# Kernel optimization log

Hardware: AMD Instinct MI355X
Metric: run time of the kernel (lower is better)

The kernel has to match this reference:

```python
import jax, jax.numpy as jnp
import numpy as np

B, N, C, OUT, K2 = 64, 4096, 64, 64, 4  # batch, lattice sites, in/out features, kersize^2

def setup_inputs() -> dict:
    key = jax.random.key(0)
    k1, k2, k3, k4 = jax.random.split(key, 4)
    std = 0.5 / jnp.sqrt(K2 * (C + OUT))  # matches module's init stddev (W_scale=b_scale=1)
    x = jax.random.normal(k1, (B, N, C), dtype=jnp.float32)
    W = jax.random.normal(k2, (K2, C, OUT), dtype=jnp.float32) * std
    b = jax.random.normal(k3, (OUT,), dtype=jnp.float32) * std
    kernel2 = jax.random.randint(k4, (N, K2), 0, N, dtype=jnp.int32)
    return {"x": x, "W": W, "b": b, "kernel2": kernel2}

def reference(x, W, b, kernel2):
    # gather neighbors: [B, N, K2, C]; contract (K2, C) with W -> [B, N, OUT]
    y = jnp.einsum('bnkc,kco->bno', x[:, kernel2, :], W)
    # bias broadcast (original used tensordot with ones([B,N]))
    return y + b
```

## Files before the change

### kernel.cpp

```cpp
#include <hip/hip_runtime.h>
#include <stdint.h>


#define N_SITES   4096
#define C_DIM     64
#define OUT_DIM   64
#define LDS_STRIDE 264

typedef __attribute__((ext_vector_type(8))) short bf16x8;
typedef __attribute__((ext_vector_type(4))) float f32x4;

__device__ __forceinline__ uint32_t pack2_bf16(float f0, float f1) {
    uint32_t u0 = __float_as_uint(f0) + 0x8000u;
    uint32_t u1 = __float_as_uint(f1) + 0x8000u;
    return __builtin_amdgcn_perm(u1, u0, 0x07060302u);
}

__global__ __launch_bounds__(256, 3)
void conv_mfma_kernel(const float* __restrict__ x, const float* __restrict__ W,
                      const float* __restrict__ bias, const int* __restrict__ kernel2,
                      float* __restrict__ out)
{
    __shared__ __align__(16) short wt[OUT_DIM * LDS_STRIDE];

    const int tid = threadIdx.x;
    const int bi  = blockIdx.x;

    const int strip = (bi & 7) + ((bi >= 2048) ? 8 : 0);
    const int group = (bi & 2047) >> 3;
    const int n0 = group * 16;
    const int b0 = strip * 4;

    const int wave = tid >> 6;
    const int lane = tid & 63;
    const int q = lane >> 4;
    const int c = lane & 15;
    const int sl = c >> 2;
    const int b  = b0 + (c & 3);

    const int n = n0 + wave * 4 + sl;
    const int4 idx = *(const int4*)(kernel2 + n * 4);
    const float* xb = x + (size_t)b * (N_SITES * C_DIM);
    const float* rp[4] = {
        xb + (size_t)idx.x * C_DIM,
        xb + (size_t)idx.y * C_DIM,
        xb + (size_t)idx.z * C_DIM,
        xb + (size_t)idx.w * C_DIM
    };

    f32x4 pay[16];
    #pragma unroll
    for (int s = 0; s < 8; ++s) {
        const float* p = rp[s >> 1] + (s & 1) * 32 + q * 8;
        pay[2*s]     = *(const f32x4*)(p);
        pay[2*s + 1] = *(const f32x4*)(p + 4);
    }

    f32x4 bias_r[4];
    #pragma unroll
    for (int t = 0; t < 4; ++t) bias_r[t] = *(const f32x4*)&bias[t*16 + q*4];

    __builtin_amdgcn_sched_barrier(0);

    {
        const int o      = tid & 63;
        const int kkbase = (tid >> 6) * 64;
        uint32_t* dst = (uint32_t*)&wt[o * LDS_STRIDE + kkbase];
        #pragma unroll
        for (int j = 0; j < 32; ++j) {
            float f0 = W[(size_t)(kkbase + 2*j    ) * OUT_DIM + o];
            float f1 = W[(size_t)(kkbase + 2*j + 1) * OUT_DIM + o];
            dst[j] = pack2_bf16(f0, f1);
        }
    }
    __syncthreads();

    f32x4 acc[4];
    #pragma unroll
    for (int t = 0; t < 4; ++t) acc[t] = (f32x4){0.f, 0.f, 0.f, 0.f};

    #pragma unroll
    for (int s = 0; s < 8; ++s) {
        bf16x8 bfrag;
        uint32_t* bp = (uint32_t*)&bfrag;
        bp[0] = pack2_bf16(pay[2*s][0],   pay[2*s][1]);
        bp[1] = pack2_bf16(pay[2*s][2],   pay[2*s][3]);
        bp[2] = pack2_bf16(pay[2*s+1][0], pay[2*s+1][1]);
        bp[3] = pack2_bf16(pay[2*s+1][2], pay[2*s+1][3]);

        const int col = s*32 + q*8;
        #pragma unroll
        for (int t = 0; t < 4; ++t) {
            bf16x8 a = *(const bf16x8*)&wt[(t*16 + c) * LDS_STRIDE + col];
            acc[t] = __builtin_amdgcn_mfma_f32_16x16x32_bf16(a, bfrag, acc[t], 0, 0, 0);
        }
    }

    float* op = out + ((size_t)b * N_SITES + n) * OUT_DIM + q * 4;
    #pragma unroll
    for (int t = 0; t < 4; ++t) {
        f32x4 v;
        #pragma unroll
        for (int r = 0; r < 4; ++r) v[r] = acc[t][r] + bias_r[t][r];
        *(f32x4*)(op + t * 16) = v;
    }
}

extern "C" void kernel_launch(void* const* d_in, const int* in_sizes, int n_in,
                              void* d_out, int out_size, void* d_ws, size_t ws_size,
                              hipStream_t stream) {
    const float* x       = (const float*)d_in[0];
    const float* W       = (const float*)d_in[1];
    const float* bias    = (const float*)d_in[2];
    const int*   kernel2 = (const int*)d_in[3];
    float* out = (float*)d_out;

    conv_mfma_kernel<<<4096, 256, 0, stream>>>(x, W, bias, kernel2, out);
}
```

Baseline: 154.3 us.

## Process four site groups per block with software-pipelined gather loads

Each block now handles 64 sites in four phases instead of 16, which amortizes the per-block W-to-bf16 LDS staging over four times more work and cuts the grid to 1024 blocks. Within each phase, the gather loads for the next half-tile are issued while the current half's MFMAs run, double-buffering through packed registers. Occupancy hint rises from 3 to 4 blocks per CU. The trade-off is fewer blocks for latency hiding and more register pressure from the pipelined payload.

```diff
diff --git a/kernel.cpp b/kernel.cpp
--- a/kernel.cpp
+++ b/kernel.cpp
@@ -6,6 +6,7 @@
 #define C_DIM     64
 #define OUT_DIM   64
 #define LDS_STRIDE 264
+#define P_PHASES  4
 
 typedef __attribute__((ext_vector_type(8))) short bf16x8;
 typedef __attribute__((ext_vector_type(4))) float f32x4;
@@ -16,7 +17,7 @@
     return __builtin_amdgcn_perm(u1, u0, 0x07060302u);
 }
 
-__global__ __launch_bounds__(256, 3)
+__global__ __launch_bounds__(256, 4)
 void conv_mfma_kernel(const float* __restrict__ x, const float* __restrict__ W,
                       const float* __restrict__ bias, const int* __restrict__ kernel2,
                       float* __restrict__ out)
@@ -26,41 +27,20 @@
     const int tid = threadIdx.x;
     const int bi  = blockIdx.x;
 
-    const int strip = (bi & 7) + ((bi >= 2048) ? 8 : 0);
-    const int group = (bi & 2047) >> 3;
-    const int n0 = group * 16;
-    const int b0 = strip * 4;
+    const int strip = (bi & 7) + ((bi >= 512) ? 8 : 0);
+    const int g     = (bi & 511) >> 3;
+    const int n0    = g * 64;
 
     const int wave = tid >> 6;
     const int lane = tid & 63;
-    const int q = lane >> 4;
-    const int c = lane & 15;
+    const int q  = lane >> 4;
+    const int c  = lane & 15;
     const int sl = c >> 2;
-    const int b  = b0 + (c & 3);
+    const int b  = strip * 4 + (c & 3);
 
-    const int n = n0 + wave * 4 + sl;
-    const int4 idx = *(const int4*)(kernel2 + n * 4);
-    const float* xb = x + (size_t)b * (N_SITES * C_DIM);
-    const float* rp[4] = {
-        xb + (size_t)idx.x * C_DIM,
-        xb + (size_t)idx.y * C_DIM,
-        xb + (size_t)idx.z * C_DIM,
-        xb + (size_t)idx.w * C_DIM
-    };
+    const int nbase = n0 + wave * 4 + sl;
 
-    f32x4 pay[16];
-    #pragma unroll
-    for (int s = 0; s < 8; ++s) {
-        const float* p = rp[s >> 1] + (s & 1) * 32 + q * 8;
-        pay[2*s]     = *(const f32x4*)(p);
-        pay[2*s + 1] = *(const f32x4*)(p + 4);
-    }
-
-    f32x4 bias_r[4];
-    #pragma unroll
-    for (int t = 0; t < 4; ++t) bias_r[t] = *(const f32x4*)&bias[t*16 + q*4];
-
-    __builtin_amdgcn_sched_barrier(0);
+    int4 idx = *(const int4*)(kernel2 + nbase * 4);
 
     {
         const int o      = tid & 63;
@@ -73,36 +53,99 @@
             dst[j] = pack2_bf16(f0, f1);
         }
     }
+
+    f32x4 bias_r[4];
+    #pragma unroll
+    for (int t = 0; t < 4; ++t) bias_r[t] = *(const f32x4*)&bias[t*16 + q*4];
+
+    const float* xq = x + (size_t)b * (N_SITES * C_DIM) + q * 8;
+
+    f32x4    pay[8];
+    uint32_t pk[16];
+    uint32_t off[4];
+
+    auto build_off = [&](int4 v) {
+        off[0] = (uint32_t)v.x * C_DIM; off[1] = (uint32_t)v.y * C_DIM;
+        off[2] = (uint32_t)v.z * C_DIM; off[3] = (uint32_t)v.w * C_DIM;
+    };
+    auto load_half = [&](int h) {
+        #pragma unroll
+        for (int s = 0; s < 4; ++s) {
+            const float* p = xq + off[h*2 + (s >> 1)] + (s & 1) * 32;
+            pay[2*s]     = *(const f32x4*)(p);
+            pay[2*s + 1] = *(const f32x4*)(p + 4);
+        }
+    };
+    auto pack_half = [&]() {
+        #pragma unroll
+        for (int s = 0; s < 4; ++s) {
+            pk[4*s+0] = pack2_bf16(pay[2*s][0],   pay[2*s][1]);
+            pk[4*s+1] = pack2_bf16(pay[2*s][2],   pay[2*s][3]);
+            pk[4*s+2] = pack2_bf16(pay[2*s+1][0], pay[2*s+1][1]);
+            pk[4*s+3] = pack2_bf16(pay[2*s+1][2], pay[2*s+1][3]);
+        }
+    };
+
+    build_off(idx);
+    load_half(0);
+    int4 idxn = *(const int4*)(kernel2 + (nbase + 16) * 4);
+
     __syncthreads();
 
-    f32x4 acc[4];
-    #pragma unroll
-    for (int t = 0; t < 4; ++t) acc[t] = (f32x4){0.f, 0.f, 0.f, 0.f};
+    pack_half();
+    load_half(1);
 
     #pragma unroll
-    for (int s = 0; s < 8; ++s) {
-        bf16x8 bfrag;
-        uint32_t* bp = (uint32_t*)&bfrag;
-        bp[0] = pack2_bf16(pay[2*s][0],   pay[2*s][1]);
-        bp[1] = pack2_bf16(pay[2*s][2],   pay[2*s][3]);
-        bp[2] = pack2_bf16(pay[2*s+1][0], pay[2*s+1][1]);
-        bp[3] = pack2_bf16(pay[2*s+1][2], pay[2*s+1][3]);
+    for (int p = 0; p < P_PHASES; ++p) {
+        const int n = nbase + p * 16;
 
-        const int col = s*32 + q*8;
+        f32x4 acc[4];
+        #pragma unroll
+        for (int t = 0; t < 4; ++t) acc[t] = (f32x4){0.f, 0.f, 0.f, 0.f};
+
+        #pragma unroll
+        for (int s = 0; s < 4; ++s) {
+            bf16x8 bf = *(const bf16x8*)&pk[4*s];
+            const int col = s*32 + q*8;
+            #pragma unroll
+            for (int t = 0; t < 4; ++t) {
+                bf16x8 a = *(const bf16x8*)&wt[(t*16 + c) * LDS_STRIDE + col];
+                acc[t] = __builtin_amdgcn_mfma_f32_16x16x32_bf16(a, bf, acc[t], 0, 0, 0);
+            }
+        }
+
+        pack_half();
+        if (p + 1 < P_PHASES) {
+            build_off(idxn);
+            load_half(0);
+        }
+        if (p + 2 < P_PHASES)
+            idxn = *(const int4*)(kernel2 + (nbase + (p + 2) * 16) * 4);
+
+        #pragma unroll
+        for (int s = 0; s < 4; ++s) {
+            bf16x8 bf = *(const bf16x8*)&pk[4*s];
+            const int col = (4 + s)*32 + q*8;
+            #pragma unroll
+            for (int t = 0; t < 4; ++t) {
+                bf16x8 a = *(const bf16x8*)&wt[(t*16 + c) * LDS_STRIDE + col];
+                acc[t] = __builtin_amdgcn_mfma_f32_16x16x32_bf16(a, bf, acc[t], 0, 0, 0);
+            }
+        }
+
+        if (p + 1 < P_PHASES) {
+            pack_half();
+            load_half(1);
+        }
+
+        float* op = out + ((size_t)b * N_SITES + n) * OUT_DIM + q * 4;
         #pragma unroll
         for (int t = 0; t < 4; ++t) {
-            bf16x8 a = *(const bf16x8*)&wt[(t*16 + c) * LDS_STRIDE + col];
-            acc[t] = __builtin_amdgcn_mfma_f32_16x16x32_bf16(a, bfrag, acc[t], 0, 0, 0);
+            f32x4 v;
+            #pragma unroll
+            for (int r = 0; r < 4; ++r) v[r] = acc[t][r] + bias_r[t][r];
+            *(f32x4*)(op + t * 16) = v;
         }
-    }
-
-    float* op = out + ((size_t)b * N_SITES + n) * OUT_DIM + q * 4;
-    #pragma unroll
-    for (int t = 0; t < 4; ++t) {
-        f32x4 v;
-        #pragma unroll
-        for (int r = 0; r < 4; ++r) v[r] = acc[t][r] + bias_r[t][r];
-        *(f32x4*)(op + t * 16) = v;
     }
 }
 
@@ -115,5 +158,5 @@
     const int*   kernel2 = (const int*)d_in[3];
     float* out = (float*)d_out;
 
-    conv_mfma_kernel<<<4096, 256, 0, stream>>>(x, W, bias, kernel2, out);
+    conv_mfma_kernel<<<1024, 256, 0, stream>>>(x, W, bias, kernel2, out);
 }
```

New measurement: 152.1 us. No clear change (-1.4%).
